# Performance work log

Measured on AMD Instinct MI355X. Metric: run time of the kernel, lower is better.

Reference implementation:

```python
import jax, jax.numpy as jnp
import numpy as np

BN_EPS = 1e-5


def setup_inputs() -> dict:
    key = jax.random.key(0)
    ks = jax.random.split(key, 10)
    B, C2, Hh, Ww = 4, 64, 64, 64  # in_channels=128, C/2=64
    C = 2 * C2
    inp = {
        "H": jax.random.normal(ks[0], (B, C2, Hh, Ww), jnp.float32),
        "L": jax.random.normal(ks[1], (B, C2, Hh, Ww), jnp.float32),
        # 1x1 convs stored as [out, in] matrices
        "theta_w": jax.random.normal(ks[2], (C2, C), jnp.float32) * (1.0 / np.sqrt(C)),
        "theta_b": jnp.zeros((C2,), jnp.float32),
        "phi_w": jax.random.normal(ks[3], (C2, C), jnp.float32) * (1.0 / np.sqrt(C)),
        "phi_b": jnp.zeros((C2,), jnp.float32),
        "g_w": jax.random.normal(ks[4], (C2, C2), jnp.float32) * (1.0 / np.sqrt(C2)),
        "g_b": jnp.zeros((C2,), jnp.float32),
        # 3x3 conv of CBR block, OIHW
        "conv_w": jax.random.normal(ks[5], (C2, C2, 3, 3), jnp.float32) * (1.0 / np.sqrt(C2 * 9)),
        "conv_b": jnp.zeros((C2,), jnp.float32),
        # BatchNorm (inference-mode) params
        "bn_gamma": jnp.ones((C2,), jnp.float32),
        "bn_beta": jnp.zeros((C2,), jnp.float32),
        "bn_mean": jnp.zeros((C2,), jnp.float32),
        "bn_var": jnp.ones((C2,), jnp.float32),
    }
    return inp


def reference(H, L, theta_w, theta_b, phi_w, phi_b, g_w, g_b,
              conv_w, conv_b, bn_gamma, bn_beta, bn_mean, bn_var):
    B, C2, h, w = L.shape
    N = h * w
    HL = jnp.concatenate([H, L], axis=1)  # [B, C, h, w]
    # 1x1 conv projections as channel matmuls
    A = jnp.einsum('oc,bchw->bohw', theta_w, HL) + theta_b[:, None, None]  # [B,C2,h,w]
    Bm = jnp.einsum('oc,bchw->bohw', phi_w, HL) + phi_b[:, None, None]
    A = A.reshape(B, C2, N).transpose(0, 2, 1)   # [B, N, C2]
    Bm = Bm.reshape(B, C2, N)                    # [B, C2, N]
    M = jnp.einsum('bnc,bcm->bnm', A, Bm)        # [B, N, N], unscaled
    M = jax.nn.softmax(M, axis=1)                # softmax over FIRST spatial axis (dim=1)
    D = jnp.einsum('oc,bchw->bohw', g_w, L) + g_b[:, None, None]
    D = D.reshape(B, C2, N)                      # [B, C2, N]
    E = jnp.einsum('bcn,bnm->bcm', D, M)         # [B, C2, N]
    E = E.reshape(B, C2, h, w)
    # CBR: conv3x3(pad=1) -> BatchNorm (inference) -> ReLU
    F = jax.lax.conv_general_dilated(
        E, conv_w, window_strides=(1, 1), padding='SAME',
        dimension_numbers=('NCHW', 'OIHW', 'NCHW')) + conv_b[None, :, None, None]
    F = (F - bn_mean[None, :, None, None]) * jax.lax.rsqrt(bn_var + BN_EPS)[None, :, None, None]
    F = F * bn_gamma[None, :, None, None] + bn_beta[None, :, None, None]
    F = jax.nn.relu(F)
    return H + F
```

## Files before the change

### kernel.cpp

```cpp
#include <hip/hip_runtime.h>

typedef __bf16 bf16;
typedef unsigned short u16;
typedef __attribute__((ext_vector_type(8))) __bf16 bf16x8;
typedef __attribute__((ext_vector_type(16))) float f32x16;
typedef __attribute__((ext_vector_type(2))) unsigned int uint2v;
typedef __attribute__((ext_vector_type(4))) unsigned int uint4v;

#define MFMA32(a, b, c) __builtin_amdgcn_mfma_f32_32x32x16_bf16(a, b, c, 0, 0, 0)

__device__ __forceinline__ u16 bbits(float f) {
  bf16 h = (bf16)f;
  return __builtin_bit_cast(u16, h);
}
__device__ __forceinline__ float bf2f(u16 u) {
  return (float)__builtin_bit_cast(bf16, u);
}
__device__ __forceinline__ bf16x8 ldg16(const u16* p) {
  return *reinterpret_cast<const bf16x8*>(p);
}
__device__ __forceinline__ bf16x8 ld_p8(const u16* p) {
  uint2v a = *reinterpret_cast<const uint2v*>(p);
  uint2v b = *reinterpret_cast<const uint2v*>(p + 4);
  uint4v u;
  u.x = a.x; u.y = a.y; u.z = b.x; u.w = b.y;
  return __builtin_bit_cast(bf16x8, u);
}
__device__ __forceinline__ unsigned packbf(float a, float b) {
  return (unsigned)bbits(a) | ((unsigned)bbits(b) << 16);
}
__device__ __forceinline__ void split8(const float* xv, bf16x8& hi, bf16x8& lo) {
  uint4v hv, lv;
#pragma unroll
  for (int jp = 0; jp < 4; ++jp) {
    float a0 = xv[2 * jp], a1 = xv[2 * jp + 1];
    u16 h0 = bbits(a0), h1 = bbits(a1);
    u16 l0 = bbits(a0 - bf2f(h0)), l1 = bbits(a1 - bf2f(h1));
    unsigned hh = (unsigned)h0 | ((unsigned)h1 << 16);
    unsigned ll = (unsigned)l0 | ((unsigned)l1 << 16);
    if (jp == 0) { hv.x = hh; lv.x = ll; }
    else if (jp == 1) { hv.y = hh; lv.y = ll; }
    else if (jp == 2) { hv.z = hh; lv.z = ll; }
    else { hv.w = hh; lv.w = ll; }
  }
  hi = __builtin_bit_cast(bf16x8, hv);
  lo = __builtin_bit_cast(bf16x8, lv);
}


__global__ __launch_bounds__(256) void pa_prep(
    const float* __restrict__ cw, const float* __restrict__ cbias,
    const float* __restrict__ gamma, const float* __restrict__ beta,
    const float* __restrict__ mean, const float* __restrict__ var,
    const float* __restrict__ tw, const float* __restrict__ pw, const float* __restrict__ gw,
    u16* __restrict__ Wt, float* __restrict__ bnA, float* __restrict__ bnB,
    u16* __restrict__ Wth, u16* __restrict__ Wtl,
    u16* __restrict__ Wph, u16* __restrict__ Wpl,
    u16* __restrict__ Wgh, u16* __restrict__ Wgl) {
  int i = blockIdx.x * 256 + threadIdx.x;
  if (i < 36864) {
    int ci = i & 63, co = (i >> 6) & 63, s = i >> 12;
    int kc = ci >> 4, q2c = (ci >> 3) & 1, j = ci & 7;
    int lane = q2c * 32 + (co & 31);
    int cbi = co >> 5;
    Wt[(((s * 4 + kc) * 2 + cbi) * 64 + lane) * 8 + j] = bbits(cw[(co * 64 + ci) * 9 + s]);
  }
  if (i < 16384) {
    int ii = i & 8191;
    int j = ii & 7, l = (ii >> 3) & 63, f = ii >> 9;
    int out = (f & 1) * 32 + (l & 31);
    int in = (f >> 1) * 16 + (l >> 5) * 8 + j;
    const float* W = (i < 8192) ? tw : pw;
    float v = W[out * 128 + in];
    u16 h = bbits(v);
    u16 lo = bbits(v - bf2f(h));
    if (i < 8192) { Wth[ii] = h; Wtl[ii] = lo; }
    else { Wph[ii] = h; Wpl[ii] = lo; }
  } else if (i < 20480) {
    int ii = i - 16384;
    int j = ii & 7, l = (ii >> 3) & 63, f = ii >> 9;
    int out = (f & 1) * 32 + (l & 31);
    int in = (f >> 1) * 16 + (l >> 5) * 8 + j;
    float v = gw[out * 64 + in];
    u16 h = bbits(v);
    Wgh[ii] = h;
    Wgl[ii] = bbits(v - bf2f(h));
  }
  if (i < 64) {
    float rs = rsqrtf(var[i] + 1e-5f);
    float A = gamma[i] * rs;
    bnA[i] = A;
    bnB[i] = (cbias[i] - mean[i]) * A + beta[i];
  }
}

template <bool LO>
__device__ __forceinline__ void store_qk_swz(const f32x16& a0, const f32x16& a1,
                                             const float* __restrict__ bias,
                                             u16* __restrict__ Hi, u16* __restrict__ Lo,
                                             int base, int l31, int q2) {
#pragma unroll
  for (int mt = 0; mt < 2; ++mt) {
    const f32x16& A = mt ? a1 : a0;
#pragma unroll
    for (int rq = 0; rq < 4; ++rq) {
      int ch = mt * 32 + rq * 8 + q2 * 4;
      float4 bb = *reinterpret_cast<const float4*>(bias + ch);
      float v0 = A[rq * 4 + 0] + bb.x;
      float v1 = A[rq * 4 + 1] + bb.y;
      float v2 = A[rq * 4 + 2] + bb.z;
      float v3 = A[rq * 4 + 3] + bb.w;
      int off = base + ((mt * 2 + (rq >> 1)) * 64 + l31 + 32 * (rq & 1)) * 8 + q2 * 4;
      u16 h0 = bbits(v0), h1 = bbits(v1), h2 = bbits(v2), h3 = bbits(v3);
      uint2v hv;
      hv.x = (unsigned)h0 | ((unsigned)h1 << 16);
      hv.y = (unsigned)h2 | ((unsigned)h3 << 16);
      *reinterpret_cast<uint2v*>(Hi + off) = hv;
      if (LO) {
        u16 l0 = bbits(v0 - bf2f(h0)), l1 = bbits(v1 - bf2f(h1));
        u16 l2 = bbits(v2 - bf2f(h2)), l3 = bbits(v3 - bf2f(h3));
        uint2v lv;
        lv.x = (unsigned)l0 | ((unsigned)l1 << 16);
        lv.y = (unsigned)l2 | ((unsigned)l3 << 16);
        *reinterpret_cast<uint2v*>(Lo + off) = lv;
      }
    }
  }
}

template <int NS>
__device__ __forceinline__ void gemm3(const u16* __restrict__ Wh, const u16* __restrict__ Wl,
                                      const bf16x8* Bh, const bf16x8* Bl,
                                      int lane, f32x16& a0, f32x16& a1) {
#pragma unroll
  for (int s = 0; s < NS; ++s) {
    bf16x8 w0h = ldg16(Wh + ((s * 2 + 0) * 64 + lane) * 8);
    bf16x8 w0l = ldg16(Wl + ((s * 2 + 0) * 64 + lane) * 8);
    bf16x8 w1h = ldg16(Wh + ((s * 2 + 1) * 64 + lane) * 8);
    bf16x8 w1l = ldg16(Wl + ((s * 2 + 1) * 64 + lane) * 8);
    a0 = MFMA32(w0h, Bh[s], a0);
    a0 = MFMA32(w0h, Bl[s], a0);
    a0 = MFMA32(w0l, Bh[s], a0);
    a1 = MFMA32(w1h, Bh[s], a1);
    a1 = MFMA32(w1h, Bl[s], a1);
    a1 = MFMA32(w1l, Bh[s], a1);
  }
}

template <int NS>
__device__ __forceinline__ void gemm2(const u16* __restrict__ Wh,
                                      const bf16x8* Bh, const bf16x8* Bl,
                                      int lane, f32x16& a0, f32x16& a1) {
#pragma unroll
  for (int s = 0; s < NS; ++s) {
    bf16x8 w0h = ldg16(Wh + ((s * 2 + 0) * 64 + lane) * 8);
    bf16x8 w1h = ldg16(Wh + ((s * 2 + 1) * 64 + lane) * 8);
    a0 = MFMA32(w0h, Bh[s], a0);
    a0 = MFMA32(w0h, Bl[s], a0);
    a1 = MFMA32(w1h, Bh[s], a1);
    a1 = MFMA32(w1h, Bl[s], a1);
  }
}

__global__ __launch_bounds__(384, 3) void pa_proj(
    const float* __restrict__ H, const float* __restrict__ L,
    const float* __restrict__ tb, const float* __restrict__ pb, const float* __restrict__ gb,
    const u16* __restrict__ Wth, const u16* __restrict__ Wph, const u16* __restrict__ Wpl,
    const u16* __restrict__ Wgh,
    u16* __restrict__ Qh, u16* __restrict__ Ql,
    u16* __restrict__ Kh, u16* __restrict__ V) {
  __shared__ float Rb[3 * 64 * 33];
  int b = blockIdx.x >> 7;
  int t = blockIdx.x & 127;
  int w = threadIdx.x >> 6;
  int lane = threadIdx.x & 63;
  int l31 = lane & 31, q2 = lane >> 5;
  int role = w >> 1, kh2 = w & 1;
  int n = t * 32 + l31;
  int base = t * 2048;

  f32x16 a0 = {}, a1 = {};
  if (role < 2) {
    bf16x8 Bh[4], Bl[4];
#pragma unroll
    for (int si = 0; si < 4; ++si) {
      int s = kh2 * 4 + si;
      const float* src = (s < 4) ? (H + (b * 64 + s * 16) * 4096)
                                 : (L + (b * 64 + (s - 4) * 16) * 4096);
      const float* pp = src + (q2 * 8) * 4096 + n;
      float xv[8];
#pragma unroll
      for (int j = 0; j < 8; ++j) xv[j] = pp[j * 4096];
      split8(xv, Bh[si], Bl[si]);
    }
    if (role == 0)
      gemm2<4>(Wth + kh2 * 4096, Bh, Bl, lane, a0, a1);
    else
      gemm3<4>(Wph + kh2 * 4096, Wpl + kh2 * 4096, Bh, Bl, lane, a0, a1);
  } else {
    bf16x8 Bh[2], Bl[2];
#pragma unroll
    for (int si = 0; si < 2; ++si) {
      int s = kh2 * 2 + si;
      const float* pp = L + (b * 64 + s * 16 + q2 * 8) * 4096 + n;
      float xv[8];
#pragma unroll
      for (int j = 0; j < 8; ++j) xv[j] = pp[j * 4096];
      split8(xv, Bh[si], Bl[si]);
    }
    gemm2<2>(Wgh + kh2 * 2048, Bh, Bl, lane, a0, a1);
  }

  float* rp = Rb + (role * 64 + lane) * 33;
  if (kh2 == 1) {
#pragma unroll
    for (int r = 0; r < 16; ++r) rp[r] = a0[r];
#pragma unroll
    for (int r = 0; r < 16; ++r) rp[16 + r] = a1[r];
  }
  __syncthreads();
  if (kh2 == 1) return;
#pragma unroll
  for (int r = 0; r < 16; ++r) a0[r] += rp[r];
#pragma unroll
  for (int r = 0; r < 16; ++r) a1[r] += rp[16 + r];

  if (role == 0) {
    store_qk_swz<false>(a0, a1, tb, Kh + b * 262144, (u16*)nullptr, base, l31, q2);
  } else if (role == 1) {
    store_qk_swz<true>(a0, a1, pb, Qh + b * 262144, Ql + b * 262144, base, l31, q2);
  } else {
    u16* Vb = V + b * 262144;
    int kch = (l31 >> 4) & 1, q2v = (l31 >> 3) & 1, jn = l31 & 7;
    (void)kch; (void)q2v; (void)jn;
#pragma unroll
    for (int mt = 0; mt < 2; ++mt) {
      const f32x16& A = mt ? a1 : a0;
#pragma unroll
      for (int rq = 0; rq < 4; ++rq) {
        int ch = mt * 32 + rq * 8 + q2 * 4;
        float4 bb = *reinterpret_cast<const float4*>(gb + ch);
        float vv[4] = {A[rq * 4 + 0] + bb.x, A[rq * 4 + 1] + bb.y,
                       A[rq * 4 + 2] + bb.z, A[rq * 4 + 3] + bb.w};
#pragma unroll
        for (int i2 = 0; i2 < 4; ++i2) {
          int c31 = rq * 8 + q2 * 4 + i2;
          int kch2 = (l31 >> 4) & 1, q2v2 = (l31 >> 3) & 1, jn2 = l31 & 7;
          int lane_v = c31 + 32 * q2v2;
          Vb[(((t * 2 + kch2) * 2 + mt) * 64 + lane_v) * 8 + jn2] = bbits(vv[i2]);
        }
      }
    }
  }
}

__global__ __launch_bounds__(512, 2) void pa_flash(
    const u16* __restrict__ Qhg, const u16* __restrict__ Qlg,
    const u16* __restrict__ Khg, const u16* __restrict__ Vg, u16* __restrict__ E) {
  __shared__ float Obuf[64 * 67];
  __shared__ float MLm[8 * 2 * 32];
  __shared__ float MLl[8 * 2 * 32];
  __shared__ float Lst[64];

  int tid = threadIdx.x;
  int w = tid >> 6, lane = tid & 63;
  int l31 = lane & 31, q2 = lane >> 5;
  int blk = blockIdx.x;
  int xcd = blk & 7;
  int b = xcd >> 1;
  int mt = ((blk >> 3) << 1) | (xcd & 1);
  int m0 = mt * 64;
  int bq = b * 4096;
  const u16* Qb = Qhg + b * 262144;
  const u16* Qlb = Qlg + b * 262144;
  const u16* Kb = Khg + b * 262144;
  const u16* Vb = Vg + b * 262144;

  bf16x8 qh[2][4], ql[2][4];
#pragma unroll
  for (int mb = 0; mb < 2; ++mb)
#pragma unroll
    for (int kc = 0; kc < 4; ++kc) {
      qh[mb][kc] = ldg16(Qb + (((mt * 2 + mb) * 4 + kc) * 64 + lane) * 8);
      ql[mb][kc] = ldg16(Qlb + (((mt * 2 + mb) * 4 + kc) * 64 + lane) * 8);
    }

  f32x16 accO[2][2] = {};
  float Mm[2] = {0.f, 0.f}, Ll[2] = {0.f, 0.f};

  bf16x8 kh[4];
#pragma unroll
  for (int kc = 0; kc < 4; ++kc) kh[kc] = ldg16(Kb + ((w * 4 + kc) * 64 + lane) * 8);

#pragma unroll 1
  for (int it = 0; it < 16; ++it) {
    int tile = it * 8 + w;

    bf16x8 vf[2][2];
#pragma unroll
    for (int kch = 0; kch < 2; ++kch)
#pragma unroll
      for (int cbi = 0; cbi < 2; ++cbi)
        vf[cbi][kch] = ldg16(Vb + (((tile * 2 + kch) * 2 + cbi) * 64 + lane) * 8);

    f32x16 s[2];
#pragma unroll
    for (int mb = 0; mb < 2; ++mb) {
      f32x16 a = {};
#pragma unroll
      for (int kc = 0; kc < 4; ++kc) {
        a = MFMA32(kh[kc], qh[mb][kc], a);
        a = MFMA32(kh[kc], ql[mb][kc], a);
      }
      s[mb] = a;
    }
    int tn = (it < 15) ? tile + 8 : tile;
#pragma unroll
    for (int kc = 0; kc < 4; ++kc) kh[kc] = ldg16(Kb + ((tn * 4 + kc) * 64 + lane) * 8);

#pragma unroll
    for (int mb = 0; mb < 2; ++mb) {
      if (it == 0) {
        float tmax = s[mb][0];
#pragma unroll
        for (int r = 1; r < 16; ++r) tmax = fmaxf(tmax, s[mb][r]);
        tmax = fmaxf(tmax, __shfl_xor(tmax, 32, 64));
        Mm[mb] = tmax;
      }
      float pv[16];
      float psum = 0.f;
#pragma unroll
      for (int r = 0; r < 16; ++r) {
        pv[r] = __expf(s[mb][r] - Mm[mb]);
        psum += pv[r];
      }
      psum += __shfl_xor(psum, 32, 64);
      Ll[mb] += psum;

      unsigned pd[4][2];
#pragma unroll
      for (int q = 0; q < 4; ++q) {
        pd[q][0] = packbf(pv[q * 4 + 0], pv[q * 4 + 1]);
        pd[q][1] = packbf(pv[q * 4 + 2], pv[q * 4 + 3]);
      }
      unsigned xd[4][2];
#pragma unroll
      for (int q = 0; q < 4; ++q) {
        xd[q][0] = (unsigned)__shfl_xor((int)pd[q][0], 32, 64);
        xd[q][1] = (unsigned)__shfl_xor((int)pd[q][1], 32, 64);
      }
      uint4v u0, u1;
      u0.x = q2 ? xd[1][0] : pd[0][0];
      u0.y = q2 ? xd[1][1] : pd[0][1];
      u0.z = q2 ? pd[1][0] : xd[0][0];
      u0.w = q2 ? pd[1][1] : xd[0][1];
      u1.x = q2 ? xd[3][0] : pd[2][0];
      u1.y = q2 ? xd[3][1] : pd[2][1];
      u1.z = q2 ? pd[3][0] : xd[2][0];
      u1.w = q2 ? pd[3][1] : xd[2][1];
      bf16x8 p0 = __builtin_bit_cast(bf16x8, u0);
      bf16x8 p1 = __builtin_bit_cast(bf16x8, u1);

      accO[0][mb] = MFMA32(vf[0][0], p0, accO[0][mb]);
      accO[0][mb] = MFMA32(vf[0][1], p1, accO[0][mb]);
      accO[1][mb] = MFMA32(vf[1][0], p0, accO[1][mb]);
      accO[1][mb] = MFMA32(vf[1][1], p1, accO[1][mb]);
    }
  }

  if (q2 == 0) {
#pragma unroll
    for (int mb = 0; mb < 2; ++mb) {
      MLm[(w * 2 + mb) * 32 + l31] = Mm[mb];
      MLl[(w * 2 + mb) * 32 + l31] = Ll[mb];
    }
  }
  __syncthreads();
  float mysc[2];
#pragma unroll
  for (int mb = 0; mb < 2; ++mb) {
    float M = MLm[mb * 32 + l31];
    for (int ww = 1; ww < 8; ++ww) M = fmaxf(M, MLm[(ww * 2 + mb) * 32 + l31]);
    float ls = 0.f;
    for (int ww = 0; ww < 8; ++ww)
      ls += MLl[(ww * 2 + mb) * 32 + l31] * __expf(MLm[(ww * 2 + mb) * 32 + l31] - M);
    mysc[mb] = __expf(Mm[mb] - M);
    if (w == 0 && q2 == 0) Lst[mb * 32 + l31] = ls;
  }
  for (int ww = 0; ww < 8; ++ww) {
    if (w == ww) {
#pragma unroll
      for (int cbi = 0; cbi < 2; ++cbi)
#pragma unroll
        for (int mb = 0; mb < 2; ++mb) {
          float sc = mysc[mb];
#pragma unroll
          for (int r = 0; r < 16; ++r) {
            int c = cbi * 32 + (r & 3) + 8 * (r >> 2) + 4 * q2;
            int m = mb * 32 + l31;
            float* dst = &Obuf[c * 67 + m];
            float v = accO[cbi][mb][r] * sc;
            if (ww == 0)
              *dst = v;
            else
              *dst += v;
          }
        }
    }
    __syncthreads();
  }
  int em = tid >> 3, ec0 = (tid & 7) * 8;
  float invl = 1.0f / Lst[em];
  float vals[8];
#pragma unroll
  for (int j = 0; j < 8; ++j) vals[j] = Obuf[(ec0 + j) * 67 + em] * invl;
  uint4v u0;
  u0.x = packbf(vals[0], vals[1]);
  u0.y = packbf(vals[2], vals[3]);
  u0.z = packbf(vals[4], vals[5]);
  u0.w = packbf(vals[6], vals[7]);
  *reinterpret_cast<uint4v*>(E + (bq + m0 + em) * 64 + ec0) = u0;
}

__global__ __launch_bounds__(512) void pa_conv(
    const u16* __restrict__ E, const u16* __restrict__ Wt,
    const float* __restrict__ bnA, const float* __restrict__ bnB,
    const float* __restrict__ H, float* __restrict__ out) {
  __shared__ u16 Er[3][66 * 68];
  __shared__ float Rbuf[4][64 * 17];
  int tid = threadIdx.x;
  int blk = blockIdx.x;
  int b = blk >> 6, y = blk & 63;
  int lane = tid & 63;
  int l31 = lane & 31, q2 = lane >> 5;
  int wv = tid >> 6;
  int ks = wv & 1, mb = (wv >> 1) & 1, cbi = wv >> 2;
  int s0 = (y == 0) ? 1 : 0;
  int s1 = (y == 63) ? 1 : 2;

  for (int s = s0; s <= s1; ++s) {
    int yy = y + s - 1;
    int x = tid >> 3, co = (tid & 7) * 8;
    const uint2v* src = reinterpret_cast<const uint2v*>(E + ((b * 4096 + yy * 64 + x) * 64 + co));
    uint2v a = src[0], b4 = src[1];
    u16* d = &Er[s][(x + 1) * 68 + co];
    *reinterpret_cast<uint2v*>(d) = a;
    *reinterpret_cast<uint2v*>(d + 4) = b4;
  }
  if (tid < 96) {
    int s = tid >> 5, side = (tid >> 4) & 1, co = (tid & 15) * 4;
    uint2v z;
    z.x = 0;
    z.y = 0;
    *reinterpret_cast<uint2v*>(&Er[s][(side ? 65 : 0) * 68 + co]) = z;
  }
  __syncthreads();

  f32x16 a0 = {}, a1 = {};
  for (int s = s0; s <= s1; ++s) {
#pragma unroll
    for (int dx = 0; dx < 3; ++dx) {
      int s3 = s * 3 + dx;
      int kcA = ks * 2, kcB = ks * 2 + 1;
      bf16x8 wa = ldg16(Wt + (((s3 * 4 + kcA) * 2 + cbi) * 64 + lane) * 8);
      bf16x8 wb = ldg16(Wt + (((s3 * 4 + kcB) * 2 + cbi) * 64 + lane) * 8);
      bf16x8 ea = ld_p8(&Er[s][(mb * 32 + l31 + dx) * 68 + kcA * 16 + q2 * 8]);
      bf16x8 eb = ld_p8(&Er[s][(mb * 32 + l31 + dx) * 68 + kcB * 16 + q2 * 8]);
      a0 = MFMA32(wa, ea, a0);
      a1 = MFMA32(wb, eb, a1);
    }
  }
  int p = cbi * 2 + mb;
  if (ks == 1) {
#pragma unroll
    for (int r = 0; r < 16; ++r) Rbuf[p][lane * 17 + r] = a0[r] + a1[r];
  }
  __syncthreads();
  if (ks == 0) {
#pragma unroll
    for (int r = 0; r < 16; ++r) {
      int c = cbi * 32 + (r & 3) + 8 * (r >> 2) + 4 * q2;
      int x = mb * 32 + l31;
      float v = a0[r] + a1[r] + Rbuf[p][lane * 17 + r];
      v = v * bnA[c] + bnB[c];
      v = fmaxf(v, 0.f);
      int idx = ((b * 64 + c) * 64 + y) * 64 + x;
      out[idx] = H[idx] + v;
    }
  }
}

extern "C" void kernel_launch(void* const* d_in, const int* in_sizes, int n_in,
                              void* d_out, int out_size, void* d_ws, size_t ws_size,
                              hipStream_t stream) {
  (void)in_sizes; (void)n_in; (void)out_size; (void)ws_size;
  const float* H = (const float*)d_in[0];
  const float* L = (const float*)d_in[1];
  const float* tw = (const float*)d_in[2];
  const float* tb = (const float*)d_in[3];
  const float* pw = (const float*)d_in[4];
  const float* pb = (const float*)d_in[5];
  const float* gw = (const float*)d_in[6];
  const float* gb = (const float*)d_in[7];
  const float* cw = (const float*)d_in[8];
  const float* cb = (const float*)d_in[9];
  const float* gamma = (const float*)d_in[10];
  const float* beta = (const float*)d_in[11];
  const float* mean = (const float*)d_in[12];
  const float* var = (const float*)d_in[13];

  const int NC = 16384 * 64;
  u16* Qh = (u16*)d_ws;
  u16* Ql = Qh + NC;
  u16* Kh = Ql + NC;
  u16* Vv = Kh + NC;
  u16* Eb = Vv + NC;
  u16* Wt = Eb + NC;
  float* bnA = (float*)(Wt + 36864);
  float* bnB = bnA + 64;
  u16* Wth = (u16*)(bnB + 64);
  u16* Wtl = Wth + 8192;
  u16* Wph = Wtl + 8192;
  u16* Wpl = Wph + 8192;
  u16* Wgh = Wpl + 8192;
  u16* Wgl = Wgh + 4096;

  pa_prep<<<144, 256, 0, stream>>>(cw, cb, gamma, beta, mean, var, tw, pw, gw,
                                   Wt, bnA, bnB, Wth, Wtl, Wph, Wpl, Wgh, Wgl);
  pa_proj<<<512, 384, 0, stream>>>(H, L, tb, pb, gb, Wth, Wph, Wpl, Wgh,
                                   Qh, Ql, Kh, Vv);
  pa_flash<<<256, 512, 0, stream>>>(Qh, Ql, Kh, Vv, Eb);
  pa_conv<<<256, 512, 0, stream>>>(Eb, Wt, bnA, bnB, H, (float*)d_out);
}
```

Measured before the change: 136.1 us.

## Fold weight prep into projection kernel and parallelize flash output reduction

Removes the separate pa_prep launch. The projection kernel now reads fp32 theta/phi/g weights directly and splits them to bf16 hi/lo in registers, and its blocks also write the conv weight layout and BN constants. The flash kernel's serialized 8-step per-warp accumulation into shared memory is replaced by four warp-pair partial buffers followed by a parallel tree sum. This saves one kernel launch and several barriers, at the cost of redundant per-block weight conversion and more shared memory in the flash kernel.

```diff
diff --git a/kernel.cpp b/kernel.cpp
--- a/kernel.cpp
+++ b/kernel.cpp
@@ -47,52 +47,6 @@
   lo = __builtin_bit_cast(bf16x8, lv);
 }
 
-
-__global__ __launch_bounds__(256) void pa_prep(
-    const float* __restrict__ cw, const float* __restrict__ cbias,
-    const float* __restrict__ gamma, const float* __restrict__ beta,
-    const float* __restrict__ mean, const float* __restrict__ var,
-    const float* __restrict__ tw, const float* __restrict__ pw, const float* __restrict__ gw,
-    u16* __restrict__ Wt, float* __restrict__ bnA, float* __restrict__ bnB,
-    u16* __restrict__ Wth, u16* __restrict__ Wtl,
-    u16* __restrict__ Wph, u16* __restrict__ Wpl,
-    u16* __restrict__ Wgh, u16* __restrict__ Wgl) {
-  int i = blockIdx.x * 256 + threadIdx.x;
-  if (i < 36864) {
-    int ci = i & 63, co = (i >> 6) & 63, s = i >> 12;
-    int kc = ci >> 4, q2c = (ci >> 3) & 1, j = ci & 7;
-    int lane = q2c * 32 + (co & 31);
-    int cbi = co >> 5;
-    Wt[(((s * 4 + kc) * 2 + cbi) * 64 + lane) * 8 + j] = bbits(cw[(co * 64 + ci) * 9 + s]);
-  }
-  if (i < 16384) {
-    int ii = i & 8191;
-    int j = ii & 7, l = (ii >> 3) & 63, f = ii >> 9;
-    int out = (f & 1) * 32 + (l & 31);
-    int in = (f >> 1) * 16 + (l >> 5) * 8 + j;
-    const float* W = (i < 8192) ? tw : pw;
-    float v = W[out * 128 + in];
-    u16 h = bbits(v);
-    u16 lo = bbits(v - bf2f(h));
-    if (i < 8192) { Wth[ii] = h; Wtl[ii] = lo; }
-    else { Wph[ii] = h; Wpl[ii] = lo; }
-  } else if (i < 20480) {
-    int ii = i - 16384;
-    int j = ii & 7, l = (ii >> 3) & 63, f = ii >> 9;
-    int out = (f & 1) * 32 + (l & 31);
-    int in = (f >> 1) * 16 + (l >> 5) * 8 + j;
-    float v = gw[out * 64 + in];
-    u16 h = bbits(v);
-    Wgh[ii] = h;
-    Wgl[ii] = bbits(v - bf2f(h));
-  }
-  if (i < 64) {
-    float rs = rsqrtf(var[i] + 1e-5f);
-    float A = gamma[i] * rs;
-    bnA[i] = A;
-    bnB[i] = (cbias[i] - mean[i]) * A + beta[i];
-  }
-}
 
 template <bool LO>
 __device__ __forceinline__ void store_qk_swz(const f32x16& a0, const f32x16& a1,
@@ -128,56 +82,53 @@
   }
 }
 
-template <int NS>
-__device__ __forceinline__ void gemm3(const u16* __restrict__ Wh, const u16* __restrict__ Wl,
-                                      const bf16x8* Bh, const bf16x8* Bl,
-                                      int lane, f32x16& a0, f32x16& a1) {
-#pragma unroll
-  for (int s = 0; s < NS; ++s) {
-    bf16x8 w0h = ldg16(Wh + ((s * 2 + 0) * 64 + lane) * 8);
-    bf16x8 w0l = ldg16(Wl + ((s * 2 + 0) * 64 + lane) * 8);
-    bf16x8 w1h = ldg16(Wh + ((s * 2 + 1) * 64 + lane) * 8);
-    bf16x8 w1l = ldg16(Wl + ((s * 2 + 1) * 64 + lane) * 8);
-    a0 = MFMA32(w0h, Bh[s], a0);
-    a0 = MFMA32(w0h, Bl[s], a0);
-    a0 = MFMA32(w0l, Bh[s], a0);
-    a1 = MFMA32(w1h, Bh[s], a1);
-    a1 = MFMA32(w1h, Bl[s], a1);
-    a1 = MFMA32(w1l, Bh[s], a1);
-  }
-}
-
-template <int NS>
-__device__ __forceinline__ void gemm2(const u16* __restrict__ Wh,
-                                      const bf16x8* Bh, const bf16x8* Bl,
-                                      int lane, f32x16& a0, f32x16& a1) {
-#pragma unroll
-  for (int s = 0; s < NS; ++s) {
-    bf16x8 w0h = ldg16(Wh + ((s * 2 + 0) * 64 + lane) * 8);
-    bf16x8 w1h = ldg16(Wh + ((s * 2 + 1) * 64 + lane) * 8);
-    a0 = MFMA32(w0h, Bh[s], a0);
-    a0 = MFMA32(w0h, Bl[s], a0);
-    a1 = MFMA32(w1h, Bh[s], a1);
-    a1 = MFMA32(w1h, Bl[s], a1);
-  }
+__device__ __forceinline__ void wfrag_f32(const float* __restrict__ W, int row, int inb,
+                                          int stride, bf16x8& h, bf16x8& l) {
+  const float* p = W + row * stride + inb;
+  float xv[8];
+  *reinterpret_cast<float4*>(xv) = *reinterpret_cast<const float4*>(p);
+  *reinterpret_cast<float4*>(xv + 4) = *reinterpret_cast<const float4*>(p + 4);
+  split8(xv, h, l);
 }
 
 __global__ __launch_bounds__(384, 3) void pa_proj(
     const float* __restrict__ H, const float* __restrict__ L,
-    const float* __restrict__ tb, const float* __restrict__ pb, const float* __restrict__ gb,
-    const u16* __restrict__ Wth, const u16* __restrict__ Wph, const u16* __restrict__ Wpl,
-    const u16* __restrict__ Wgh,
+    const float* __restrict__ tw, const float* __restrict__ tb,
+    const float* __restrict__ pw, const float* __restrict__ pb,
+    const float* __restrict__ gw, const float* __restrict__ gb,
+    const float* __restrict__ cw, const float* __restrict__ cbias,
+    const float* __restrict__ gamma, const float* __restrict__ beta,
+    const float* __restrict__ mean, const float* __restrict__ var,
     u16* __restrict__ Qh, u16* __restrict__ Ql,
-    u16* __restrict__ Kh, u16* __restrict__ V) {
+    u16* __restrict__ Kh, u16* __restrict__ V,
+    u16* __restrict__ Wt, float* __restrict__ bnA, float* __restrict__ bnB) {
   __shared__ float Rb[3 * 64 * 33];
+  int tid = threadIdx.x;
   int b = blockIdx.x >> 7;
   int t = blockIdx.x & 127;
-  int w = threadIdx.x >> 6;
-  int lane = threadIdx.x & 63;
+  int w = tid >> 6;
+  int lane = tid & 63;
   int l31 = lane & 31, q2 = lane >> 5;
   int role = w >> 1, kh2 = w & 1;
   int n = t * 32 + l31;
   int base = t * 2048;
+
+  {
+    int gid = blockIdx.x * 384 + tid;
+    if (gid < 36864) {
+      int j = gid & 7, ln = (gid >> 3) & 63, cbi = (gid >> 9) & 1;
+      int kc = (gid >> 10) & 3, s = gid >> 12;
+      int co = cbi * 32 + (ln & 31);
+      int ci = kc * 16 + ((ln >> 5) & 1) * 8 + j;
+      Wt[gid] = bbits(cw[(co * 64 + ci) * 9 + s]);
+    } else if (gid < 36928) {
+      int c = gid - 36864;
+      float rs = rsqrtf(var[c] + 1e-5f);
+      float A = gamma[c] * rs;
+      bnA[c] = A;
+      bnB[c] = (cbias[c] - mean[c]) * A + beta[c];
+    }
+  }
 
   f32x16 a0 = {}, a1 = {};
   if (role < 2) {
@@ -193,10 +144,22 @@
       for (int j = 0; j < 8; ++j) xv[j] = pp[j * 4096];
       split8(xv, Bh[si], Bl[si]);
     }
-    if (role == 0)
-      gemm2<4>(Wth + kh2 * 4096, Bh, Bl, lane, a0, a1);
-    else
-      gemm3<4>(Wph + kh2 * 4096, Wpl + kh2 * 4096, Bh, Bl, lane, a0, a1);
+    const float* W = role ? pw : tw;
+#pragma unroll
+    for (int si = 0; si < 4; ++si) {
+      int inb = (kh2 * 4 + si) * 16 + q2 * 8;
+      bf16x8 w0h, w0l, w1h, w1l;
+      wfrag_f32(W, l31, inb, 128, w0h, w0l);
+      wfrag_f32(W, 32 + l31, inb, 128, w1h, w1l);
+      a0 = MFMA32(w0h, Bh[si], a0);
+      a0 = MFMA32(w0h, Bl[si], a0);
+      a1 = MFMA32(w1h, Bh[si], a1);
+      a1 = MFMA32(w1h, Bl[si], a1);
+      if (role == 1) {
+        a0 = MFMA32(w0l, Bh[si], a0);
+        a1 = MFMA32(w1l, Bh[si], a1);
+      }
+    }
   } else {
     bf16x8 Bh[2], Bl[2];
 #pragma unroll
@@ -208,7 +171,17 @@
       for (int j = 0; j < 8; ++j) xv[j] = pp[j * 4096];
       split8(xv, Bh[si], Bl[si]);
     }
-    gemm2<2>(Wgh + kh2 * 2048, Bh, Bl, lane, a0, a1);
+#pragma unroll
+    for (int si = 0; si < 2; ++si) {
+      int inb = (kh2 * 2 + si) * 16 + q2 * 8;
+      bf16x8 w0h, w0l, w1h, w1l;
+      wfrag_f32(gw, l31, inb, 64, w0h, w0l);
+      wfrag_f32(gw, 32 + l31, inb, 64, w1h, w1l);
+      a0 = MFMA32(w0h, Bh[si], a0);
+      a0 = MFMA32(w0h, Bl[si], a0);
+      a1 = MFMA32(w1h, Bh[si], a1);
+      a1 = MFMA32(w1h, Bl[si], a1);
+    }
   }
 
   float* rp = Rb + (role * 64 + lane) * 33;
@@ -232,7 +205,6 @@
   } else {
     u16* Vb = V + b * 262144;
     int kch = (l31 >> 4) & 1, q2v = (l31 >> 3) & 1, jn = l31 & 7;
-    (void)kch; (void)q2v; (void)jn;
 #pragma unroll
     for (int mt = 0; mt < 2; ++mt) {
       const f32x16& A = mt ? a1 : a0;
@@ -245,9 +217,8 @@
 #pragma unroll
         for (int i2 = 0; i2 < 4; ++i2) {
           int c31 = rq * 8 + q2 * 4 + i2;
-          int kch2 = (l31 >> 4) & 1, q2v2 = (l31 >> 3) & 1, jn2 = l31 & 7;
-          int lane_v = c31 + 32 * q2v2;
-          Vb[(((t * 2 + kch2) * 2 + mt) * 64 + lane_v) * 8 + jn2] = bbits(vv[i2]);
+          int lane_v = c31 + 32 * q2v;
+          Vb[(((t * 2 + kch) * 2 + mt) * 64 + lane_v) * 8 + jn] = bbits(vv[i2]);
         }
       }
     }
@@ -257,7 +228,7 @@
 __global__ __launch_bounds__(512, 2) void pa_flash(
     const u16* __restrict__ Qhg, const u16* __restrict__ Qlg,
     const u16* __restrict__ Khg, const u16* __restrict__ Vg, u16* __restrict__ E) {
-  __shared__ float Obuf[64 * 67];
+  __shared__ float Reg[4][64 * 65];
   __shared__ float MLm[8 * 2 * 32];
   __shared__ float MLl[8 * 2 * 32];
   __shared__ float Lst[64];
@@ -387,33 +358,49 @@
     mysc[mb] = __expf(Mm[mb] - M);
     if (w == 0 && q2 == 0) Lst[mb * 32 + l31] = ls;
   }
-  for (int ww = 0; ww < 8; ++ww) {
-    if (w == ww) {
-#pragma unroll
-      for (int cbi = 0; cbi < 2; ++cbi)
-#pragma unroll
-        for (int mb = 0; mb < 2; ++mb) {
-          float sc = mysc[mb];
-#pragma unroll
-          for (int r = 0; r < 16; ++r) {
-            int c = cbi * 32 + (r & 3) + 8 * (r >> 2) + 4 * q2;
-            int m = mb * 32 + l31;
-            float* dst = &Obuf[c * 67 + m];
-            float v = accO[cbi][mb][r] * sc;
-            if (ww == 0)
-              *dst = v;
-            else
-              *dst += v;
-          }
+  if (w >= 4) {
+    float* R = Reg[w - 4];
+#pragma unroll
+    for (int cbi = 0; cbi < 2; ++cbi)
+#pragma unroll
+      for (int mb = 0; mb < 2; ++mb) {
+        float sc = mysc[mb];
+#pragma unroll
+        for (int r = 0; r < 16; ++r) {
+          int c = cbi * 32 + (r & 3) + 8 * (r >> 2) + 4 * q2;
+          int m = mb * 32 + l31;
+          R[c * 65 + m] = accO[cbi][mb][r] * sc;
         }
-    }
-    __syncthreads();
-  }
+      }
+  }
+  __syncthreads();
+  if (w < 4) {
+    float* R = Reg[w];
+#pragma unroll
+    for (int cbi = 0; cbi < 2; ++cbi)
+#pragma unroll
+      for (int mb = 0; mb < 2; ++mb) {
+        float sc = mysc[mb];
+#pragma unroll
+        for (int r = 0; r < 16; ++r) {
+          int c = cbi * 32 + (r & 3) + 8 * (r >> 2) + 4 * q2;
+          int m = mb * 32 + l31;
+          R[c * 65 + m] += accO[cbi][mb][r] * sc;
+        }
+      }
+  }
+  __syncthreads();
+  for (int i = tid; i < 4096; i += 512) {
+    int c = i >> 6, m = i & 63;
+    int a = c * 65 + m;
+    Reg[0][a] = (Reg[0][a] + Reg[1][a]) + (Reg[2][a] + Reg[3][a]);
+  }
+  __syncthreads();
   int em = tid >> 3, ec0 = (tid & 7) * 8;
   float invl = 1.0f / Lst[em];
   float vals[8];
 #pragma unroll
-  for (int j = 0; j < 8; ++j) vals[j] = Obuf[(ec0 + j) * 67 + em] * invl;
+  for (int j = 0; j < 8; ++j) vals[j] = Reg[0][(ec0 + j) * 65 + em] * invl;
   uint4v u0;
   u0.x = packbf(vals[0], vals[1]);
   u0.y = packbf(vals[2], vals[3]);
@@ -518,17 +505,10 @@
   u16* Wt = Eb + NC;
   float* bnA = (float*)(Wt + 36864);
   float* bnB = bnA + 64;
-  u16* Wth = (u16*)(bnB + 64);
-  u16* Wtl = Wth + 8192;
-  u16* Wph = Wtl + 8192;
-  u16* Wpl = Wph + 8192;
-  u16* Wgh = Wpl + 8192;
-  u16* Wgl = Wgh + 4096;
-
-  pa_prep<<<144, 256, 0, stream>>>(cw, cb, gamma, beta, mean, var, tw, pw, gw,
-                                   Wt, bnA, bnB, Wth, Wtl, Wph, Wpl, Wgh, Wgl);
-  pa_proj<<<512, 384, 0, stream>>>(H, L, tb, pb, gb, Wth, Wph, Wpl, Wgh,
-                                   Qh, Ql, Kh, Vv);
+
+  pa_proj<<<512, 384, 0, stream>>>(H, L, tw, tb, pw, pb, gw, gb,
+                                   cw, cb, gamma, beta, mean, var,
+                                   Qh, Ql, Kh, Vv, Wt, bnA, bnB);
   pa_flash<<<256, 512, 0, stream>>>(Qh, Ql, Kh, Vv, Eb);
   pa_conv<<<256, 512, 0, stream>>>(Eb, Wt, bnA, bnB, H, (float*)d_out);
 }
```

Result: no change. 134.8 us (-1.0%).
